# Performance work log

Hardware: AMD Instinct MI355X
Metric: run time of the kernel (lower is better)

Reference implementation:

```python
import jax, jax.numpy as jnp
import numpy as np

BN_EPS = 1e-5


def _bn(x, gamma, beta):
    # training-mode BatchNorm1d: biased batch stats over the edge/batch axis
    mean = jnp.mean(x, axis=0, keepdims=True)
    var = jnp.mean((x - mean) ** 2, axis=0, keepdims=True)
    return (x - mean) * jax.lax.rsqrt(var + BN_EPS) * gamma + beta


def setup_inputs() -> dict:
    key = jax.random.key(0)
    ks = jax.random.split(key, 20)
    N, E = 20000, 300000
    in_drug, in_prot, hidden = 256, 512, 256
    h2 = 2 * hidden

    def u(k, shape, fan_in):
        b = 1.0 / np.sqrt(fan_in)
        return jax.random.uniform(k, shape, jnp.float32, -b, b)

    return {
        "x_drug": jax.random.normal(ks[0], (N, in_drug), jnp.float32),
        "x_prot": jax.random.normal(ks[1], (N, in_prot), jnp.float32),
        "edge_index": jax.random.randint(ks[2], (2, E), 0, N, jnp.int64),
        "W_src": u(ks[3], (hidden, in_drug), in_drug),
        "W_dst": u(ks[4], (hidden, in_prot), in_prot),
        "W_gate": u(ks[5], (h2, h2), h2),
        "b_gate": u(ks[6], (h2,), h2),
        "W1": u(ks[7], (hidden, h2), h2),
        "b1": u(ks[8], (hidden,), h2),
        "g1": jnp.ones((hidden,), jnp.float32),
        "be1": jnp.zeros((hidden,), jnp.float32),
        "W2": u(ks[9], (hidden, hidden), hidden),
        "b2": u(ks[10], (hidden,), hidden),
        "g2": jnp.ones((hidden,), jnp.float32),
        "be2": jnp.zeros((hidden,), jnp.float32),
        "W3": u(ks[11], (1, hidden), hidden),
        "b3": u(ks[12], (1,), hidden),
        "W_bil": u(ks[13], (1, hidden, hidden), hidden),
        "b_bil": u(ks[14], (1,), hidden),
    }


def reference(x_drug, x_prot, edge_index, W_src, W_dst, W_gate, b_gate,
              W1, b1, g1, be1, W2, b2, g2, be2, W3, b3, W_bil, b_bil):
    src, dst = edge_index[0], edge_index[1]
    h_src = x_drug[src] @ W_src.T            # [E, H]
    h_dst = x_prot[dst] @ W_dst.T            # [E, H]
    h_cat = jnp.concatenate([h_src, h_dst], axis=1)  # [E, 2H]
    gate = jax.nn.sigmoid(h_cat @ W_gate.T + b_gate)
    h = gate * h_cat
    # MLP (dropout is identity here)
    h1 = jax.nn.relu(_bn(h @ W1.T + b1, g1, be1))
    h2_ = jax.nn.relu(_bn(h1 @ W2.T + b2, g2, be2))
    mlp_score = (h2_ @ W3.T + b3).reshape(-1)
    # Bilinear: out_ek = sum_ij h_src_ei W_kij h_dst_ej + b_k
    bil_score = (jnp.einsum("ei,kij,ej->ek", h_src, W_bil, h_dst) + b_bil).reshape(-1)
    return mlp_score + bil_score
```

## Files before the change

### kernel.cpp

```cpp
#include <hip/hip_runtime.h>
#include <hip/hip_bf16.h>

typedef unsigned short u16;
typedef __attribute__((ext_vector_type(8))) short bf16x8;
typedef __attribute__((ext_vector_type(8))) unsigned short us8;
typedef __attribute__((ext_vector_type(4))) float f32x4;


__device__ __forceinline__ float b2f(u16 u) {
    union { unsigned u32; float f; } x; x.u32 = ((unsigned)u) << 16; return x.f;
}
__device__ __forceinline__ u16 f2b(float f) {
    union { float f; unsigned u; } x; x.f = f;
    unsigned r = x.u + 0x7fffu + ((x.u >> 16) & 1u);
    return (u16)(r >> 16);
}

__global__ __launch_bounds__(256) void zero_kernel(float* p, int n) {
    int i = blockIdx.x * 256 + threadIdx.x;
    if (i < n) p[i] = 0.f;
}

struct CvtSeg { const float* in; u16* out; int n4; };
struct CvtArr { CvtSeg s[6]; int tot4; };
__global__ __launch_bounds__(256) void cvt_fused(CvtArr ca) {
    int i = blockIdx.x * 256 + threadIdx.x;
    if (i >= ca.tot4) return;
    int k = 0, off = i;
#pragma unroll
    for (int q = 0; q < 6; ++q) {
        if (off < ca.s[q].n4) { k = q; break; }
        off -= ca.s[q].n4;
    }
    float4 v = ((const float4*)ca.s[k].in)[off];
    ushort4 o; o.x = f2b(v.x); o.y = f2b(v.y); o.z = f2b(v.z); o.w = f2b(v.w);
    ((ushort4*)ca.s[k].out)[off] = o;
}

struct GDesc {
    const void* A; int lda; int a_f32;
    const u16* W; int ldb;
    u16* C; int ldc;
    int K;
    const float* bias;
};
template <int NY> struct GDescArr { GDesc d[NY]; };

template <int NY>
__global__ __launch_bounds__(256, 2) void mfma_node(GDescArr<NY> da, int M)
{
    const GDesc dd = da.d[blockIdx.y];
    __shared__ u16 As[2][128][40];
    __shared__ u16 Bs[2][256][40];
    const int t = threadIdx.x;
    const int row0 = blockIdx.x * 128;
    const int arow = t >> 1, aks = (t & 1) * 16;
    const int agr = min(row0 + arow, M - 1);
    const int w = t >> 6, lane = t & 63;
    const int wr = w >> 1, wc = w & 1;
    const int lrow = lane & 15, lkg = lane >> 4;
    const int NIT = dd.K >> 5;

    f32x4 acc[4][8] = {};
    us8 ar[2], br[4];
    float4 fr[4];

    auto load_regs = [&](int it) {
        const int k0 = it << 5;
        if (dd.a_f32) {
            const float* ap = (const float*)dd.A + (size_t)agr * dd.lda + k0 + aks;
#pragma unroll
            for (int q = 0; q < 4; ++q) fr[q] = *(const float4*)(ap + q * 4);
        } else {
            const u16* ap = (const u16*)dd.A + (size_t)agr * dd.lda + k0 + aks;
            ar[0] = *(const us8*)ap; ar[1] = *(const us8*)(ap + 8);
        }
        const u16* wp = dd.W + (size_t)t * dd.ldb + k0;
#pragma unroll
        for (int q = 0; q < 4; ++q) br[q] = *(const us8*)(wp + q * 8);
    };
    auto proc_write = [&](int b) {
        if (dd.a_f32) {
#pragma unroll
            for (int q = 0; q < 2; ++q) {
                us8 o;
                const float fq[8] = {fr[q*2].x, fr[q*2].y, fr[q*2].z, fr[q*2].w,
                                     fr[q*2+1].x, fr[q*2+1].y, fr[q*2+1].z, fr[q*2+1].w};
#pragma unroll
                for (int j = 0; j < 8; ++j) o[j] = f2b(fq[j]);
                *(us8*)&As[b][arow][aks + q * 8] = o;
            }
        } else {
            *(us8*)&As[b][arow][aks] = ar[0];
            *(us8*)&As[b][arow][aks + 8] = ar[1];
        }
#pragma unroll
        for (int q = 0; q < 4; ++q) *(us8*)&Bs[b][t][q * 8] = br[q];
    };
    auto do_mfma = [&](int b) {
        bf16x8 af[4];
#pragma unroll
        for (int mi = 0; mi < 4; ++mi)
            af[mi] = *(const bf16x8*)&As[b][wr * 64 + mi * 16 + lrow][lkg * 8];
#pragma unroll
        for (int ni = 0; ni < 8; ++ni) {
            bf16x8 bfr = *(const bf16x8*)&Bs[b][wc * 128 + ni * 16 + lrow][lkg * 8];
#pragma unroll
            for (int mi = 0; mi < 4; ++mi)
                acc[mi][ni] = __builtin_amdgcn_mfma_f32_16x16x32_bf16(
                    af[mi], bfr, acc[mi][ni], 0, 0, 0);
        }
    };

    load_regs(0); proc_write(0); __syncthreads();
    for (int it = 0; it < NIT; ++it) {
        const int cur = it & 1;
        if (it + 1 < NIT) load_regs(it + 1);
        do_mfma(cur);
        if (it + 1 < NIT) proc_write(cur ^ 1);
        __syncthreads();
    }

#pragma unroll
    for (int ni = 0; ni < 8; ++ni) {
        const int gcol = wc * 128 + ni * 16 + lrow;
        const float bv = dd.bias ? dd.bias[gcol] : 0.f;
#pragma unroll
        for (int mi = 0; mi < 4; ++mi) {
            f32x4 v = acc[mi][ni];
#pragma unroll
            for (int j = 0; j < 4; ++j) {
                const int grow = row0 + wr * 64 + mi * 16 + lkg * 4 + j;
                if (grow < M) dd.C[(size_t)grow * dd.ldc + gcol] = f2b(v[j] + bv);
            }
        }
    }
}

#define OP_GATE   1
#define OP_BNRELU 2

template <int AOP>
__global__ __launch_bounds__(256, 2) void mfma_edge(
    const u16* __restrict__ Ain,
    const u16* __restrict__ Wb, int ldb, int K,
    u16* __restrict__ C, int E,
    const int* __restrict__ ei,
    const u16* __restrict__ Gs, const u16* __restrict__ Gd,
    const u16* __restrict__ Hs, const u16* __restrict__ Hd,
    const u16* __restrict__ Bd, const float* __restrict__ b_bil,
    float* __restrict__ bil,
    const float* __restrict__ scaleK, const float* __restrict__ shiftK,
    float* __restrict__ sums)
{
    __shared__ u16 As[2][128][40];
    __shared__ u16 Bs[2][256][40];
    __shared__ float wsum[2][2][256];
    __shared__ int sx[128], dx[128];

    const int t = threadIdx.x;
    const int row0 = blockIdx.x * 128;

    if constexpr (AOP == OP_GATE) {
        if (t < 128) {
            const int e = min(row0 + t, E - 1);
            sx[t] = ei[e]; dx[t] = ei[E + e];
        }
        __syncthreads();
    }

    const int arow = t >> 1, aks = (t & 1) * 16;
    const int agr = min(row0 + arow, E - 1);
    const int w = t >> 6, lane = t & 63;
    const int wr = w >> 1, wc = w & 1;
    const int lrow = lane & 15, lkg = lane >> 4;
    const int NIT = K >> 5;

    f32x4 acc[4][8] = {};
    float bdot = 0.f;
    us8 g1r[2], g2r[2], hr[2], bdr[2], br[4];
    float4 scA[2], scB[2], shA[2], shB[2];

    auto load_regs = [&](int it) {
        const int k0 = it << 5;
        const int kg = k0 + aks;
        if constexpr (AOP == OP_GATE) {
            const int s = sx[arow], d = dx[arow];
            const u16* gsp = Gs + (size_t)s * 512 + kg;
            const u16* gdp = Gd + (size_t)d * 512 + kg;
            g1r[0] = *(const us8*)gsp; g1r[1] = *(const us8*)(gsp + 8);
            g2r[0] = *(const us8*)gdp; g2r[1] = *(const us8*)(gdp + 8);
            const u16* hp = (k0 < 256) ? (Hs + (size_t)s * 256 + kg)
                                       : (Hd + (size_t)d * 256 + kg - 256);
            hr[0] = *(const us8*)hp; hr[1] = *(const us8*)(hp + 8);
            if (k0 < 256) {
                const u16* bp = Bd + (size_t)dx[arow] * 256 + kg;
                bdr[0] = *(const us8*)bp; bdr[1] = *(const us8*)(bp + 8);
            }
        } else {
            const u16* ap = Ain + (size_t)agr * 256 + kg;
            g1r[0] = *(const us8*)ap; g1r[1] = *(const us8*)(ap + 8);
#pragma unroll
            for (int q = 0; q < 2; ++q) {
                scA[q] = *(const float4*)(scaleK + kg + q * 8);
                scB[q] = *(const float4*)(scaleK + kg + q * 8 + 4);
                shA[q] = *(const float4*)(shiftK + kg + q * 8);
                shB[q] = *(const float4*)(shiftK + kg + q * 8 + 4);
            }
        }
        const u16* wp = Wb + (size_t)t * ldb + k0;
#pragma unroll
        for (int q = 0; q < 4; ++q) br[q] = *(const us8*)(wp + q * 8);
    };
    auto proc_write = [&](int it, int b) {
        const int k0 = it << 5;
#pragma unroll
        for (int q = 0; q < 2; ++q) {
            us8 o;
            if constexpr (AOP == OP_GATE) {
#pragma unroll
                for (int j = 0; j < 8; ++j) {
                    const float x = b2f(g1r[q][j]) + b2f(g2r[q][j]);
                    const float g = 1.f / (1.f + __expf(-x));
                    o[j] = f2b(g * b2f(hr[q][j]));
                }
                if (k0 < 256) {
#pragma unroll
                    for (int j = 0; j < 8; ++j)
                        bdot = fmaf(b2f(hr[q][j]), b2f(bdr[q][j]), bdot);
                }
            } else {
                const float scq[8] = {scA[q].x, scA[q].y, scA[q].z, scA[q].w,
                                      scB[q].x, scB[q].y, scB[q].z, scB[q].w};
                const float shq[8] = {shA[q].x, shA[q].y, shA[q].z, shA[q].w,
                                      shB[q].x, shB[q].y, shB[q].z, shB[q].w};
#pragma unroll
                for (int j = 0; j < 8; ++j)
                    o[j] = f2b(fmaxf(fmaf(b2f(g1r[q][j]), scq[j], shq[j]), 0.f));
            }
            *(us8*)&As[b][arow][aks + q * 8] = o;
        }
#pragma unroll
        for (int q = 0; q < 4; ++q) *(us8*)&Bs[b][t][q * 8] = br[q];
    };
    auto do_mfma = [&](int b) {
        bf16x8 af[4];
#pragma unroll
        for (int mi = 0; mi < 4; ++mi)
            af[mi] = *(const bf16x8*)&As[b][wr * 64 + mi * 16 + lrow][lkg * 8];
#pragma unroll
        for (int ni = 0; ni < 8; ++ni) {
            bf16x8 bfr = *(const bf16x8*)&Bs[b][wc * 128 + ni * 16 + lrow][lkg * 8];
#pragma unroll
            for (int mi = 0; mi < 4; ++mi)
                acc[mi][ni] = __builtin_amdgcn_mfma_f32_16x16x32_bf16(
                    af[mi], bfr, acc[mi][ni], 0, 0, 0);
        }
    };

    load_regs(0); proc_write(0, 0); __syncthreads();
    for (int it = 0; it < NIT; ++it) {
        const int cur = it & 1;
        if (it + 1 < NIT) load_regs(it + 1);
        do_mfma(cur);
        if (it + 1 < NIT) proc_write(it + 1, cur ^ 1);
        __syncthreads();
    }

    if constexpr (AOP == OP_GATE) {
        bdot += __shfl_xor(bdot, 1, 64);
        if ((t & 1) == 0 && row0 + arow < E)
            bil[row0 + arow] = bdot + b_bil[0];
    }

#pragma unroll
    for (int ni = 0; ni < 8; ++ni) {
        const int gcol = wc * 128 + ni * 16 + lrow;
        float s = 0.f, ss = 0.f;
#pragma unroll
        for (int mi = 0; mi < 4; ++mi) {
            f32x4 v = acc[mi][ni];
#pragma unroll
            for (int j = 0; j < 4; ++j) {
                const int grow = row0 + wr * 64 + mi * 16 + lkg * 4 + j;
                const float x = v[j];
                if (grow < E) {
                    C[(size_t)grow * 256 + gcol] = f2b(x);
                    s += x; ss = fmaf(x, x, ss);
                }
            }
        }
        s  += __shfl_xor(s, 16, 64);  s  += __shfl_xor(s, 32, 64);
        ss += __shfl_xor(ss, 16, 64); ss += __shfl_xor(ss, 32, 64);
        if (lkg == 0) {
            wsum[0][wr][gcol] = s;
            wsum[1][wr][gcol] = ss;
        }
    }
    __syncthreads();
    atomicAdd(&sums[t],       wsum[0][0][t] + wsum[0][1][t]);
    atomicAdd(&sums[256 + t], wsum[1][0][t] + wsum[1][1][t]);
}

__global__ void finalize_kernel(
    const float* __restrict__ sums, const float* __restrict__ g,
    const float* __restrict__ be, int M,
    float* __restrict__ scale, float* __restrict__ shift)
{
    const int c = threadIdx.x;
    const float inv = 1.f / (float)M;
    const float mean = sums[c] * inv;
    const float var  = sums[256 + c] * inv - mean * mean;
    const float sc = g[c] * rsqrtf(var + 1e-5f);
    scale[c] = sc;
    shift[c] = fmaf(-mean, sc, be[c]);
}

__global__ __launch_bounds__(256) void final_kernel(
    const u16* __restrict__ Z2,
    const float* __restrict__ scale2, const float* __restrict__ shift2,
    const float* __restrict__ W3, const float* __restrict__ b3,
    const float* __restrict__ bil,
    float* __restrict__ out, int E)
{
    const int w = threadIdx.x >> 6, lane = threadIdx.x & 63;
    const int e = blockIdx.x * 4 + w;
    if (e >= E) return;
    ushort4 zv = *(const ushort4*)(Z2 + (size_t)e * 256 + lane * 4);
    float4 sc = *(const float4*)(scale2 + lane * 4);
    float4 sh = *(const float4*)(shift2 + lane * 4);
    float4 w3 = *(const float4*)(W3 + lane * 4);
    const u16 zq[4] = {zv.x, zv.y, zv.z, zv.w};
    const float scq[4] = {sc.x, sc.y, sc.z, sc.w};
    const float shq[4] = {sh.x, sh.y, sh.z, sh.w};
    const float wq[4] = {w3.x, w3.y, w3.z, w3.w};
    float acc = 0.f;
#pragma unroll
    for (int i = 0; i < 4; ++i) {
        const float x = fmaxf(fmaf(b2f(zq[i]), scq[i], shq[i]), 0.f);
        acc = fmaf(x, wq[i], acc);
    }
#pragma unroll
    for (int off = 32; off; off >>= 1) acc += __shfl_down(acc, off, 64);
    if (lane == 0) out[e] = acc + b3[0] + bil[e];
}

extern "C" void kernel_launch(void* const* d_in, const int* in_sizes, int n_in,
                              void* d_out, int out_size, void* d_ws, size_t ws_size,
                              hipStream_t stream)
{
    const float* x_drug = (const float*)d_in[0];
    const float* x_prot = (const float*)d_in[1];
    const int*   ei     = (const int*)d_in[2];
    const float* W_src  = (const float*)d_in[3];
    const float* W_dst  = (const float*)d_in[4];
    const float* W_gate = (const float*)d_in[5];
    const float* b_gate = (const float*)d_in[6];
    const float* W1     = (const float*)d_in[7];
    const float* g1     = (const float*)d_in[9];
    const float* be1    = (const float*)d_in[10];
    const float* W2     = (const float*)d_in[11];
    const float* g2     = (const float*)d_in[13];
    const float* be2    = (const float*)d_in[14];
    const float* W3     = (const float*)d_in[15];
    const float* b3     = (const float*)d_in[16];
    const float* W_bil  = (const float*)d_in[17];
    const float* b_bil  = (const float*)d_in[18];
    float* out = (float*)d_out;

    const int N = in_sizes[0] / 256;
    const int E = in_sizes[2] / 2;

    char* wp_ = (char*)d_ws;
    auto alloc = [&](size_t bytes) {
        char* p = wp_; wp_ += (bytes + 255) & ~(size_t)255; return p;
    };
    u16* Wsrcb  = (u16*)alloc(256 * 256 * 2);
    u16* Wdstb  = (u16*)alloc(256 * 512 * 2);
    u16* Wgateb = (u16*)alloc(512 * 512 * 2);
    u16* Wbilb  = (u16*)alloc(256 * 256 * 2);
    u16* W1b    = (u16*)alloc(256 * 512 * 2);
    u16* W2b    = (u16*)alloc(256 * 256 * 2);
    u16* Hs     = (u16*)alloc((size_t)N * 256 * 2);
    u16* Hd     = (u16*)alloc((size_t)N * 256 * 2);
    u16* Gs     = (u16*)alloc((size_t)N * 512 * 2);
    u16* Gd     = (u16*)alloc((size_t)N * 512 * 2);
    u16* Bd     = (u16*)alloc((size_t)N * 256 * 2);
    u16* z      = (u16*)alloc((size_t)E * 256 * 2);
    float* bil  = (float*)alloc((size_t)E * 4);
    float* sums   = (float*)alloc(1024 * 4);
    float* scale1 = (float*)alloc(256 * 4);
    float* shift1 = (float*)alloc(256 * 4);
    float* scale2 = (float*)alloc(256 * 4);
    float* shift2 = (float*)alloc(256 * 4);

    zero_kernel<<<4, 256, 0, stream>>>(sums, 1024);

    CvtArr ca;
    ca.s[0] = {W_src,  Wsrcb,  256 * 256 / 4};
    ca.s[1] = {W_dst,  Wdstb,  256 * 512 / 4};
    ca.s[2] = {W_gate, Wgateb, 512 * 512 / 4};
    ca.s[3] = {W_bil,  Wbilb,  256 * 256 / 4};
    ca.s[4] = {W1,     W1b,    256 * 512 / 4};
    ca.s[5] = {W2,     W2b,    256 * 256 / 4};
    ca.tot4 = 0;
    for (int q = 0; q < 6; ++q) ca.tot4 += ca.s[q].n4;
    cvt_fused<<<(ca.tot4 + 255) / 256, 256, 0, stream>>>(ca);

    const int gxN = (N + 127) / 128;
    const int gxE = (E + 127) / 128;

    GDescArr<2> p1;
    p1.d[0] = {x_drug, 256, 1, Wsrcb, 256, Hs, 256, 256, nullptr};
    p1.d[1] = {x_prot, 512, 1, Wdstb, 512, Hd, 256, 512, nullptr};
    mfma_node<2><<<dim3(gxN, 2), 256, 0, stream>>>(p1, N);

    GDescArr<5> p2;
    p2.d[0] = {Hs, 256, 0, Wgateb,                 512, Gs,       512, 256, b_gate};
    p2.d[1] = {Hs, 256, 0, Wgateb + 256 * 512,     512, Gs + 256, 512, 256, b_gate + 256};
    p2.d[2] = {Hd, 256, 0, Wgateb + 256,           512, Gd,       512, 256, nullptr};
    p2.d[3] = {Hd, 256, 0, Wgateb + 256 * 512 + 256, 512, Gd + 256, 512, 256, nullptr};
    p2.d[4] = {Hd, 256, 0, Wbilb,                  256, Bd,       256, 256, nullptr};
    mfma_node<5><<<dim3(gxN, 5), 256, 0, stream>>>(p2, N);

    mfma_edge<OP_GATE><<<gxE, 256, 0, stream>>>(
        nullptr, W1b, 512, 512, z, E,
        ei, Gs, Gd, Hs, Hd, Bd, b_bil, bil, nullptr, nullptr, sums);
    finalize_kernel<<<1, 256, 0, stream>>>(sums, g1, be1, E, scale1, shift1);

    mfma_edge<OP_BNRELU><<<gxE, 256, 0, stream>>>(
        z, W2b, 256, 256, z, E,
        nullptr, nullptr, nullptr, nullptr, nullptr, nullptr, nullptr, nullptr,
        scale1, shift1, sums + 512);
    finalize_kernel<<<1, 256, 0, stream>>>(sums + 512, g2, be2, E, scale2, shift2);

    final_kernel<<<(E + 3) / 4, 256, 0, stream>>>(
        z, scale2, shift2, W3, b3, bil, out, E);
}
```

Measured before the change: 588.9 us.

## Shrink edge GEMM tile to 64 rows and read weights directly from global

The edge MFMA kernel now uses 64-row tiles, with four waves each covering 64 output columns, instead of 128-row tiles split over a 2x2 wave grid. The weight (B) operand is no longer staged through shared memory; each wave loads its MFMA fragments straight from global memory (relying on L2/L1 caching). The edge index lookups move from shared arrays into registers. This cuts LDS use and register pressure so occupancy can rise (launch bounds go from 2 to 3 blocks), at the cost of more global weight traffic per output and less reuse of each weight fragment.

```diff
diff --git a/kernel.cpp b/kernel.cpp
--- a/kernel.cpp
+++ b/kernel.cpp
@@ -141,7 +141,7 @@
 #define OP_BNRELU 2
 
 template <int AOP>
-__global__ __launch_bounds__(256, 2) void mfma_edge(
+__global__ __launch_bounds__(256, 3) void mfma_edge(
     const u16* __restrict__ Ain,
     const u16* __restrict__ Wb, int ldb, int K,
     u16* __restrict__ C, int E,
@@ -153,136 +153,118 @@
     const float* __restrict__ scaleK, const float* __restrict__ shiftK,
     float* __restrict__ sums)
 {
-    __shared__ u16 As[2][128][40];
-    __shared__ u16 Bs[2][256][40];
-    __shared__ float wsum[2][2][256];
-    __shared__ int sx[128], dx[128];
+    __shared__ u16 As[2][64][36];
+    __shared__ float wsum[2][256];
 
     const int t = threadIdx.x;
-    const int row0 = blockIdx.x * 128;
-
+    const int row0 = blockIdx.x * 64;
+    const int arow = t >> 2;
+    const int aks = (t & 3) * 8;
+    const int agr = min(row0 + arow, E - 1);
+
+    int s_ = 0, d_ = 0;
     if constexpr (AOP == OP_GATE) {
-        if (t < 128) {
-            const int e = min(row0 + t, E - 1);
-            sx[t] = ei[e]; dx[t] = ei[E + e];
-        }
-        __syncthreads();
-    }
-
-    const int arow = t >> 1, aks = (t & 1) * 16;
-    const int agr = min(row0 + arow, E - 1);
-    const int w = t >> 6, lane = t & 63;
-    const int wr = w >> 1, wc = w & 1;
+        s_ = ei[agr]; d_ = ei[E + agr];
+    }
+
+    const int lane = t & 63;
+    const int wc = t >> 6;
     const int lrow = lane & 15, lkg = lane >> 4;
     const int NIT = K >> 5;
 
-    f32x4 acc[4][8] = {};
+    f32x4 acc[4][4] = {};
     float bdot = 0.f;
-    us8 g1r[2], g2r[2], hr[2], bdr[2], br[4];
-    float4 scA[2], scB[2], shA[2], shB[2];
+    us8 g1r, g2r, hr, bdr;
+    float4 sc0, sc1, sh0, sh1;
 
     auto load_regs = [&](int it) {
         const int k0 = it << 5;
         const int kg = k0 + aks;
         if constexpr (AOP == OP_GATE) {
-            const int s = sx[arow], d = dx[arow];
-            const u16* gsp = Gs + (size_t)s * 512 + kg;
-            const u16* gdp = Gd + (size_t)d * 512 + kg;
-            g1r[0] = *(const us8*)gsp; g1r[1] = *(const us8*)(gsp + 8);
-            g2r[0] = *(const us8*)gdp; g2r[1] = *(const us8*)(gdp + 8);
-            const u16* hp = (k0 < 256) ? (Hs + (size_t)s * 256 + kg)
-                                       : (Hd + (size_t)d * 256 + kg - 256);
-            hr[0] = *(const us8*)hp; hr[1] = *(const us8*)(hp + 8);
+            g1r = *(const us8*)(Gs + (size_t)s_ * 512 + kg);
+            g2r = *(const us8*)(Gd + (size_t)d_ * 512 + kg);
+            hr = (k0 < 256) ? *(const us8*)(Hs + (size_t)s_ * 256 + kg)
+                            : *(const us8*)(Hd + (size_t)d_ * 256 + kg - 256);
+            if (k0 < 256) bdr = *(const us8*)(Bd + (size_t)d_ * 256 + kg);
+        } else {
+            g1r = *(const us8*)(Ain + (size_t)agr * 256 + kg);
+            sc0 = *(const float4*)(scaleK + kg);
+            sc1 = *(const float4*)(scaleK + kg + 4);
+            sh0 = *(const float4*)(shiftK + kg);
+            sh1 = *(const float4*)(shiftK + kg + 4);
+        }
+    };
+    auto proc_write = [&](int it, int b) {
+        const int k0 = it << 5;
+        us8 o;
+        if constexpr (AOP == OP_GATE) {
+#pragma unroll
+            for (int j = 0; j < 8; ++j) {
+                const float x = b2f(g1r[j]) + b2f(g2r[j]);
+                const float g = 1.f / (1.f + __expf(-x));
+                o[j] = f2b(g * b2f(hr[j]));
+            }
             if (k0 < 256) {
-                const u16* bp = Bd + (size_t)dx[arow] * 256 + kg;
-                bdr[0] = *(const us8*)bp; bdr[1] = *(const us8*)(bp + 8);
+#pragma unroll
+                for (int j = 0; j < 8; ++j)
+                    bdot = fmaf(b2f(hr[j]), b2f(bdr[j]), bdot);
             }
         } else {
-            const u16* ap = Ain + (size_t)agr * 256 + kg;
-            g1r[0] = *(const us8*)ap; g1r[1] = *(const us8*)(ap + 8);
-#pragma unroll
-            for (int q = 0; q < 2; ++q) {
-                scA[q] = *(const float4*)(scaleK + kg + q * 8);
-                scB[q] = *(const float4*)(scaleK + kg + q * 8 + 4);
-                shA[q] = *(const float4*)(shiftK + kg + q * 8);
-                shB[q] = *(const float4*)(shiftK + kg + q * 8 + 4);
-            }
-        }
-        const u16* wp = Wb + (size_t)t * ldb + k0;
-#pragma unroll
-        for (int q = 0; q < 4; ++q) br[q] = *(const us8*)(wp + q * 8);
-    };
-    auto proc_write = [&](int it, int b) {
+            const float scq[8] = {sc0.x, sc0.y, sc0.z, sc0.w,
+                                  sc1.x, sc1.y, sc1.z, sc1.w};
+            const float shq[8] = {sh0.x, sh0.y, sh0.z, sh0.w,
+                                  sh1.x, sh1.y, sh1.z, sh1.w};
+#pragma unroll
+            for (int j = 0; j < 8; ++j)
+                o[j] = f2b(fmaxf(fmaf(b2f(g1r[j]), scq[j], shq[j]), 0.f));
+        }
+        *(us8*)&As[b][arow][aks] = o;
+    };
+    auto do_iter = [&](int it, int b) {
         const int k0 = it << 5;
-#pragma unroll
-        for (int q = 0; q < 2; ++q) {
-            us8 o;
-            if constexpr (AOP == OP_GATE) {
-#pragma unroll
-                for (int j = 0; j < 8; ++j) {
-                    const float x = b2f(g1r[q][j]) + b2f(g2r[q][j]);
-                    const float g = 1.f / (1.f + __expf(-x));
-                    o[j] = f2b(g * b2f(hr[q][j]));
-                }
-                if (k0 < 256) {
-#pragma unroll
-                    for (int j = 0; j < 8; ++j)
-                        bdot = fmaf(b2f(hr[q][j]), b2f(bdr[q][j]), bdot);
-                }
-            } else {
-                const float scq[8] = {scA[q].x, scA[q].y, scA[q].z, scA[q].w,
-                                      scB[q].x, scB[q].y, scB[q].z, scB[q].w};
-                const float shq[8] = {shA[q].x, shA[q].y, shA[q].z, shA[q].w,
-                                      shB[q].x, shB[q].y, shB[q].z, shB[q].w};
-#pragma unroll
-                for (int j = 0; j < 8; ++j)
-                    o[j] = f2b(fmaxf(fmaf(b2f(g1r[q][j]), scq[j], shq[j]), 0.f));
-            }
-            *(us8*)&As[b][arow][aks + q * 8] = o;
-        }
-#pragma unroll
-        for (int q = 0; q < 4; ++q) *(us8*)&Bs[b][t][q * 8] = br[q];
-    };
-    auto do_mfma = [&](int b) {
+        bf16x8 bfr[4];
+#pragma unroll
+        for (int ni = 0; ni < 4; ++ni)
+            bfr[ni] = *(const bf16x8*)(Wb +
+                (size_t)(wc * 64 + ni * 16 + lrow) * ldb + k0 + lkg * 8);
         bf16x8 af[4];
 #pragma unroll
         for (int mi = 0; mi < 4; ++mi)
-            af[mi] = *(const bf16x8*)&As[b][wr * 64 + mi * 16 + lrow][lkg * 8];
-#pragma unroll
-        for (int ni = 0; ni < 8; ++ni) {
-            bf16x8 bfr = *(const bf16x8*)&Bs[b][wc * 128 + ni * 16 + lrow][lkg * 8];
+            af[mi] = *(const bf16x8*)&As[b][mi * 16 + lrow][lkg * 8];
+#pragma unroll
+        for (int ni = 0; ni < 4; ++ni)
 #pragma unroll
             for (int mi = 0; mi < 4; ++mi)
                 acc[mi][ni] = __builtin_amdgcn_mfma_f32_16x16x32_bf16(
-                    af[mi], bfr, acc[mi][ni], 0, 0, 0);
-        }
+                    af[mi], bfr[ni], acc[mi][ni], 0, 0, 0);
     };
 
     load_regs(0); proc_write(0, 0); __syncthreads();
     for (int it = 0; it < NIT; ++it) {
         const int cur = it & 1;
         if (it + 1 < NIT) load_regs(it + 1);
-        do_mfma(cur);
+        do_iter(it, cur);
         if (it + 1 < NIT) proc_write(it + 1, cur ^ 1);
         __syncthreads();
     }
 
     if constexpr (AOP == OP_GATE) {
         bdot += __shfl_xor(bdot, 1, 64);
-        if ((t & 1) == 0 && row0 + arow < E)
+        bdot += __shfl_xor(bdot, 2, 64);
+        if ((t & 3) == 0 && row0 + arow < E)
             bil[row0 + arow] = bdot + b_bil[0];
     }
 
 #pragma unroll
-    for (int ni = 0; ni < 8; ++ni) {
-        const int gcol = wc * 128 + ni * 16 + lrow;
+    for (int ni = 0; ni < 4; ++ni) {
+        const int gcol = wc * 64 + ni * 16 + lrow;
         float s = 0.f, ss = 0.f;
 #pragma unroll
         for (int mi = 0; mi < 4; ++mi) {
             f32x4 v = acc[mi][ni];
 #pragma unroll
             for (int j = 0; j < 4; ++j) {
-                const int grow = row0 + wr * 64 + mi * 16 + lkg * 4 + j;
+                const int grow = row0 + mi * 16 + lkg * 4 + j;
                 const float x = v[j];
                 if (grow < E) {
                     C[(size_t)grow * 256 + gcol] = f2b(x);
@@ -292,14 +274,11 @@
         }
         s  += __shfl_xor(s, 16, 64);  s  += __shfl_xor(s, 32, 64);
         ss += __shfl_xor(ss, 16, 64); ss += __shfl_xor(ss, 32, 64);
-        if (lkg == 0) {
-            wsum[0][wr][gcol] = s;
-            wsum[1][wr][gcol] = ss;
-        }
+        if (lkg == 0) { wsum[0][gcol] = s; wsum[1][gcol] = ss; }
     }
     __syncthreads();
-    atomicAdd(&sums[t],       wsum[0][0][t] + wsum[0][1][t]);
-    atomicAdd(&sums[256 + t], wsum[1][0][t] + wsum[1][1][t]);
+    atomicAdd(&sums[t],       wsum[0][t]);
+    atomicAdd(&sums[256 + t], wsum[1][t]);
 }
 
 __global__ void finalize_kernel(
@@ -408,7 +387,7 @@
     cvt_fused<<<(ca.tot4 + 255) / 256, 256, 0, stream>>>(ca);
 
     const int gxN = (N + 127) / 128;
-    const int gxE = (E + 127) / 128;
+    const int gxE = (E + 63) / 64;
 
     GDescArr<2> p1;
     p1.d[0] = {x_drug, 256, 1, Wsrcb, 256, Hs, 256, 256, nullptr};
```

Measured after the change: 630.4 us. 1.07x slower.
